# Optimization experiments

Hardware: AMD Instinct MI355X
Metric: run time of the kernel (lower is better)

The kernel has to match this reference:

```python
import jax, jax.numpy as jnp
import numpy as np

N = 100000   # nodes
E = 3200000  # edges (avg degree 32)
WIDTH = 32
DEPTH = 4


def setup_inputs() -> dict:
    key = jax.random.key(0)
    ks = jax.random.split(key, 12)
    def lin(k, fan_in, fan_out):
        s = 1.0 / np.sqrt(fan_in)
        kw, kb = jax.random.split(k)
        W = jax.random.uniform(kw, (fan_in, fan_out), jnp.float32, -s, s)
        b = jax.random.uniform(kb, (fan_out,), jnp.float32, -s, s)
        return W, b
    x = jax.random.normal(ks[0], (N, 3), jnp.float32)
    edge_index = jax.random.randint(ks[1], (2, E), 0, N, jnp.int64)
    fc1_w, fc1_b = lin(ks[2], 3, WIDTH)
    w1, b1 = lin(ks[3], WIDTH, 2 * WIDTH)
    w2, b2 = lin(ks[4], 2 * WIDTH, 2 * WIDTH)
    w3, b3 = lin(ks[5], 2 * WIDTH, WIDTH)
    fc2_w, fc2_b = lin(ks[6], WIDTH, 1)
    return {"x": x, "edge_index": edge_index,
            "fc1_w": fc1_w, "fc1_b": fc1_b,
            "w1": w1, "b1": b1, "w2": w2, "b2": b2, "w3": w3, "b3": b3,
            "fc2_w": fc2_w, "fc2_b": fc2_b}


def reference(x, edge_index, fc1_w, fc1_b, w1, b1, w2, b2, w3, b3, fc2_w, fc2_b):
    # GCNConv semantics: add self-loops, symmetric degree normalization,
    # linear transform then normalized scatter-add aggregation.
    loops = jnp.arange(N, dtype=edge_index.dtype)
    src = jnp.concatenate([edge_index[0], loops])  # [E+N]
    dst = jnp.concatenate([edge_index[1], loops])  # [E+N]
    deg = jax.ops.segment_sum(jnp.ones_like(dst, dtype=x.dtype), dst, num_segments=N)
    dinv = jnp.where(deg > 0, jax.lax.rsqrt(deg), 0.0)
    norm = (dinv[src] * dinv[dst])[:, None]  # [E+N, 1]

    def gcn(h, W, b):
        m = (h @ W)[src] * norm                      # gather + scale
        return jax.ops.segment_sum(m, dst, num_segments=N) + b  # scatter-add

    h = x @ fc1_w + fc1_b
    for _ in range(DEPTH):
        h = jax.nn.relu(gcn(h, w1, b1))
        h = jax.nn.relu(gcn(h, w2, b2))
        h = jax.nn.relu(gcn(h, w3, b3))
    return h @ fc2_w + fc2_b
```

## Files before the change

### kernel.cpp

```cpp
#include <hip/hip_runtime.h>
#include <hip/hip_fp16.h>

constexpr int NN = 100000;
constexpr int EE = 3200000;
constexpr int BLOCK = 256;
constexpr int NBINS = 782;
constexpr int BINCAP = 5120;
constexpr int CHUNK = 4096;
constexpr int NCHB = (EE + CHUNK - 1) / CHUNK;
constexpr int NCLS = 512;

typedef _Float16 h2v __attribute__((ext_vector_type(2)));

__device__ __forceinline__ float addLo(float acc, unsigned int bits) {
#if __has_builtin(__builtin_amdgcn_fdot2)
  h2v h = __builtin_bit_cast(h2v, bits);
  const h2v eLo = {(_Float16)1.0f, (_Float16)0.0f};
  return __builtin_amdgcn_fdot2(h, eLo, acc, false);
#else
  __half2 hh = __builtin_bit_cast(__half2, bits);
  return acc + __half2float(hh.x);
#endif
}

__device__ __forceinline__ float addHi(float acc, unsigned int bits) {
#if __has_builtin(__builtin_amdgcn_fdot2)
  h2v h = __builtin_bit_cast(h2v, bits);
  const h2v eHi = {(_Float16)0.0f, (_Float16)1.0f};
  return __builtin_amdgcn_fdot2(h, eHi, acc, false);
#else
  __half2 hh = __builtin_bit_cast(__half2, bits);
  return acc + __half2float(hh.y);
#endif
}

__global__ __launch_bounds__(256) void k_binA(const int* __restrict__ src,
                                              const int* __restrict__ dst,
                                              int* __restrict__ cursor,
                                              unsigned int* __restrict__ binarr) {
  __shared__ int cnt[1024];
  __shared__ int off[1024];
  __shared__ int gbase[NBINS];
  __shared__ int ssc[256];
  __shared__ unsigned int stag[CHUNK];
  int tid = threadIdx.x;
  int base = blockIdx.x * CHUNK;
  for (int i = tid; i < 1024; i += 256) cnt[i] = 0;
  __syncthreads();
  for (int i = tid; i < CHUNK; i += 256) {
    int e = base + i;
    if (e < EE) atomicAdd(&cnt[dst[e] >> 7], 1);
  }
  __syncthreads();
  int t4 = tid * 4;
  int s0 = cnt[t4], s1 = cnt[t4 + 1], s2 = cnt[t4 + 2], s3 = cnt[t4 + 3];
  int tsum = s0 + s1 + s2 + s3;
  ssc[tid] = tsum;
  __syncthreads();
  for (int o = 1; o < 256; o <<= 1) {
    int x = (tid >= o) ? ssc[tid - o] : 0;
    __syncthreads();
    ssc[tid] += x;
    __syncthreads();
  }
  int ex = ssc[tid] - tsum;
  off[t4] = ex;
  off[t4 + 1] = ex + s0;
  off[t4 + 2] = ex + s0 + s1;
  off[t4 + 3] = ex + s0 + s1 + s2;
  __syncthreads();
  for (int b = tid; b < NBINS; b += 256) {
    int c = cnt[b];
    gbase[b] = c ? atomicAdd(&cursor[b], c) : 0;
    cnt[b] = off[b];
  }
  __syncthreads();
  for (int i = tid; i < CHUNK; i += 256) {
    int e = base + i;
    if (e < EE) {
      int d = dst[e];
      int b = d >> 7;
      int p = atomicAdd(&cnt[b], 1);
      stag[p] = ((unsigned int)src[e] << 7) | (unsigned int)(d & 127);
    }
  }
  __syncthreads();
  int total = (base + CHUNK <= EE) ? CHUNK : (EE - base);
  for (int i = tid; i < total; i += 256) {
    int lo = 0, hi = NBINS - 1;
    while (lo < hi) {
      int mid = (lo + hi + 1) >> 1;
      if (off[mid] <= i) lo = mid;
      else hi = mid - 1;
    }
    binarr[(size_t)lo * BINCAP + gbase[lo] + (i - off[lo])] = stag[i];
  }
}

__global__ __launch_bounds__(256) void k_degcnt(const unsigned int* __restrict__ binarr,
                                                const int* __restrict__ cursor,
                                                int* __restrict__ deg,
                                                int* __restrict__ bh) {
  __shared__ int cnt[128];
  __shared__ int lh[NCLS];
  int b = blockIdx.x, tid = threadIdx.x;
  if (tid < 128) cnt[tid] = 0;
  for (int i = tid; i < NCLS; i += 256) lh[i] = 0;
  __syncthreads();
  int n = cursor[b];
  const unsigned int* p = binarr + (size_t)b * BINCAP;
  for (int i = tid; i < n; i += 256) atomicAdd(&cnt[p[i] & 127], 1);
  __syncthreads();
  int node = b * 128 + tid;
  if (tid < 128 && node < NN) {
    int d = cnt[tid] < NCLS ? cnt[tid] : NCLS - 1;
    deg[node] = d;
    atomicAdd(&lh[d], 1);
  }
  __syncthreads();
  for (int i = tid; i < NCLS; i += 256) bh[(size_t)i * NBINS + b] = lh[i];
}

__global__ __launch_bounds__(256) void k_rowscan(int* __restrict__ bh,
                                                 int* __restrict__ tot) {
  int wid = (blockIdx.x * 256 + threadIdx.x) >> 6;
  int lane = threadIdx.x & 63;
  if (wid >= NCLS) return;
  int* row = bh + (size_t)wid * NBINS;
  int run = 0;
  for (int base = 0; base < NBINS; base += 64) {
    int i = base + lane;
    int v = (i < NBINS) ? row[i] : 0;
    int s = v;
#pragma unroll
    for (int o = 1; o < 64; o <<= 1) {
      int x = __shfl_up(s, o);
      if (lane >= o) s += x;
    }
    if (i < NBINS) row[i] = run + s - v;
    run += __shfl(s, 63);
  }
  if (lane == 0) tot[wid] = run;
}

__global__ __launch_bounds__(NCLS) void k_clsscan(const int* __restrict__ tot,
                                                  int* __restrict__ nodestart,
                                                  int* __restrict__ edgebase) {
  __shared__ int sn[NCLS], se[NCLS];
  int t = threadIdx.x;
  int v = tot[t];
  int e0 = v * t;
  sn[t] = v;
  se[t] = e0;
  __syncthreads();
  for (int o = 1; o < NCLS; o <<= 1) {
    int a = 0, b = 0;
    if (t >= o) { a = sn[t - o]; b = se[t - o]; }
    __syncthreads();
    if (t >= o) { sn[t] += a; se[t] += b; }
    __syncthreads();
  }
  nodestart[t] = sn[t] - v;
  edgebase[t] = se[t] - e0;
}

__global__ __launch_bounds__(256) void k_place2(const int* __restrict__ deg,
                                                const int* __restrict__ bh,
                                                const int* __restrict__ nodestart,
                                                const int* __restrict__ edgebase,
                                                int* __restrict__ perm,
                                                int* __restrict__ invp,
                                                int* __restrict__ rowptr2,
                                                float* __restrict__ dinv2) {
  __shared__ int lcur[NCLS];
  int tid = threadIdx.x, b = blockIdx.x;
  for (int i = tid; i < NCLS; i += 256)
    lcur[i] = nodestart[i] + bh[(size_t)i * NBINS + b];
  __syncthreads();
  int n = b * 128 + tid;
  if (tid >= 128 || n >= NN) return;
  int d = deg[n];
  int nid = atomicAdd(&lcur[d], 1);
  perm[nid] = n;
  invp[n] = nid;
  int idx = nid - nodestart[d];
  rowptr2[nid] = edgebase[d] + idx * d;
  dinv2[nid] = rsqrtf((float)(d + 1));
  if (n == 0) rowptr2[NN] = EE;
}

__global__ __launch_bounds__(256) void k_binB2(const unsigned int* __restrict__ binarr,
                                               const int* __restrict__ cursor,
                                               const int* __restrict__ deg,
                                               const int* __restrict__ invp,
                                               const int* __restrict__ rowptr2,
                                               int* __restrict__ col2) {
  __shared__ int off[128];
  __shared__ int cur[128];
  __shared__ int nbase[128];
  __shared__ unsigned int stag[BINCAP];
  int b = blockIdx.x, tid = threadIdx.x;
  int node = b * 128 + tid;
  int d = 0;
  if (tid < 128) {
    d = (node < NN) ? deg[node] : 0;
    off[tid] = d;
  }
  __syncthreads();
  for (int o = 1; o < 128; o <<= 1) {
    int x = 0;
    if (tid < 128 && tid >= o) x = off[tid - o];
    __syncthreads();
    if (tid < 128) off[tid] += x;
    __syncthreads();
  }
  int ex = 0;
  if (tid < 128) ex = off[tid] - d;
  __syncthreads();
  if (tid < 128) {
    off[tid] = ex;
    cur[tid] = ex;
    nbase[tid] = (node < NN) ? rowptr2[invp[node]] : 0;
  }
  __syncthreads();
  int n = cursor[b];
  const unsigned int* p = binarr + (size_t)b * BINCAP;
  for (int i = tid; i < n; i += 256) {
    unsigned int e = p[i];
    int pos = atomicAdd(&cur[e & 127], 1);
    stag[pos] = e;
  }
  __syncthreads();
  for (int i = tid; i < n; i += 256) {
    unsigned int e = stag[i];
    int dl = e & 127;
    col2[nbase[dl] + (i - off[dl])] = invp[e >> 7];
  }
}

__global__ __launch_bounds__(BLOCK) void k_fc1(const float* __restrict__ x,
                                               __half* __restrict__ t0,
                                               const float* __restrict__ W,
                                               const float* __restrict__ b,
                                               const float* __restrict__ dinv,
                                               const int* __restrict__ perm) {
  __shared__ float Ws[3 * 32];
  __shared__ float bs[32];
  int tid = threadIdx.x;
  if (tid < 96) Ws[tid] = W[tid];
  if (tid < 32) bs[tid] = b[tid];
  __syncthreads();
  int node = blockIdx.x * 8 + (tid >> 5);
  int f = tid & 31;
  if (node >= NN) return;
  int on = perm[node];
  float x0 = x[on * 3], x1 = x[on * 3 + 1], x2 = x[on * 3 + 2];
  float v = fmaf(x0, Ws[f], fmaf(x1, Ws[32 + f], fmaf(x2, Ws[64 + f], bs[f])));
  t0[node * 32 + f] = __float2half(v * dinv[node]);
}

__global__ __launch_bounds__(BLOCK) void k_A(const uint2* __restrict__ t0,
                                             __half2* __restrict__ t1,
                                             const int* __restrict__ rowptr,
                                             const int* __restrict__ col,
                                             const float* __restrict__ dinv,
                                             const float* __restrict__ W1,
                                             const float* __restrict__ b1) {
  __shared__ __half2 W1h[32 * 32];
  __shared__ float b1s[64];
  __shared__ float Hs[32 * 33];
  int tid = threadIdx.x;
  for (int i = tid; i < 32 * 32; i += BLOCK) {
    int k = i >> 5, m = i & 31;
    W1h[i] = __floats2half2_rn(W1[k * 64 + 2 * m], W1[k * 64 + 2 * m + 1]);
  }
  if (tid < 64) b1s[tid] = b1[tid];
  __syncthreads();

  int tile = blockIdx.x;
  {
    int c = tid & 7, slot = tid >> 3;
    int node = tile * 32 + slot;
    uint2 raw = t0[(size_t)node * 8 + c];
    float a0 = 0.f, a1 = 0.f, a2 = 0.f, a3 = 0.f;
    a0 = addLo(a0, raw.x); a1 = addHi(a1, raw.x);
    a2 = addLo(a2, raw.y); a3 = addHi(a3, raw.y);
    int beg = rowptr[node], end = rowptr[node + 1];
#pragma unroll 8
    for (int e = beg; e < end; ++e) {
      uint2 r = t0[(size_t)col[e] * 8 + c];
      a0 = addLo(a0, r.x); a1 = addHi(a1, r.x);
      a2 = addLo(a2, r.y); a3 = addHi(a3, r.y);
    }
    float dv = dinv[node];
    Hs[slot * 33 + 4 * c] = a0 * dv;
    Hs[slot * 33 + 4 * c + 1] = a1 * dv;
    Hs[slot * 33 + 4 * c + 2] = a2 * dv;
    Hs[slot * 33 + 4 * c + 3] = a3 * dv;
  }
  __syncthreads();
  {
    int n = tid >> 3, c8 = tid & 7;
    int node = tile * 32 + n;
    float a[8];
#pragma unroll
    for (int j = 0; j < 8; ++j) a[j] = b1s[c8 * 8 + j];
#pragma unroll
    for (int k = 0; k < 32; ++k) {
      float h = Hs[n * 33 + k];
#pragma unroll
      for (int jj = 0; jj < 4; ++jj) {
        float2 w = __half22float2(W1h[k * 32 + c8 * 4 + jj]);
        a[2 * jj] = fmaf(h, w.x, a[2 * jj]);
        a[2 * jj + 1] = fmaf(h, w.y, a[2 * jj + 1]);
      }
    }
    float dv = dinv[node];
    __half2* o = t1 + (size_t)node * 32 + c8 * 4;
#pragma unroll
    for (int jj = 0; jj < 4; ++jj)
      o[jj] = __float22half2_rn(make_float2(fmaxf(a[2 * jj], 0.f) * dv,
                                            fmaxf(a[2 * jj + 1], 0.f) * dv));
  }
}

__global__ __launch_bounds__(BLOCK) void k_C(const uint2* __restrict__ t1,
                                             __half2* __restrict__ t3,
                                             const int* __restrict__ rowptr,
                                             const int* __restrict__ col,
                                             const float* __restrict__ dinv,
                                             const float* __restrict__ W2,
                                             const float* __restrict__ b2,
                                             const float* __restrict__ W3) {
  __shared__ __half2 W2h[64 * 32];
  __shared__ __half2 W3h[64 * 16];
  __shared__ float b2s[64];
  __shared__ float H2[16 * 65];
  __shared__ float G1[16 * 65];
  int tid = threadIdx.x;
  for (int i = tid; i < 64 * 32; i += BLOCK) {
    int k = i >> 5, m = i & 31;
    W2h[i] = __floats2half2_rn(W2[k * 64 + 2 * m], W2[k * 64 + 2 * m + 1]);
  }
  for (int i = tid; i < 64 * 16; i += BLOCK) {
    int k = i >> 4, m = i & 15;
    W3h[i] = __floats2half2_rn(W3[k * 32 + 2 * m], W3[k * 32 + 2 * m + 1]);
  }
  if (tid < 64) b2s[tid] = b2[tid];
  __syncthreads();

  int tile = blockIdx.x;
  {
    int c = tid & 15, slot = tid >> 4;
    int node = tile * 16 + slot;
    uint2 raw = t1[(size_t)node * 16 + c];
    float a0 = 0.f, a1 = 0.f, a2 = 0.f, a3 = 0.f;
    a0 = addLo(a0, raw.x); a1 = addHi(a1, raw.x);
    a2 = addLo(a2, raw.y); a3 = addHi(a3, raw.y);
    int beg = rowptr[node], end = rowptr[node + 1];
#pragma unroll 8
    for (int e = beg; e < end; ++e) {
      uint2 r = t1[(size_t)col[e] * 16 + c];
      a0 = addLo(a0, r.x); a1 = addHi(a1, r.x);
      a2 = addLo(a2, r.y); a3 = addHi(a3, r.y);
    }
    float dv = dinv[node];
    H2[slot * 65 + 4 * c] = a0 * dv;
    H2[slot * 65 + 4 * c + 1] = a1 * dv;
    H2[slot * 65 + 4 * c + 2] = a2 * dv;
    H2[slot * 65 + 4 * c + 3] = a3 * dv;
  }
  __syncthreads();
  {
    int n = tid >> 4, q = tid & 15;
    float a[4];
#pragma unroll
    for (int j = 0; j < 4; ++j) a[j] = b2s[q * 4 + j];
#pragma unroll
    for (int k = 0; k < 64; ++k) {
      float h = H2[n * 65 + k];
      float2 w0 = __half22float2(W2h[k * 32 + q * 2]);
      float2 w1 = __half22float2(W2h[k * 32 + q * 2 + 1]);
      a[0] = fmaf(h, w0.x, a[0]);
      a[1] = fmaf(h, w0.y, a[1]);
      a[2] = fmaf(h, w1.x, a[2]);
      a[3] = fmaf(h, w1.y, a[3]);
    }
#pragma unroll
    for (int j = 0; j < 4; ++j) G1[n * 65 + q * 4 + j] = fmaxf(a[j], 0.f);
  }
  __syncthreads();
  {
    int n = tid >> 4, c16 = tid & 15;
    int node = tile * 16 + n;
    float a0 = 0.f, a1 = 0.f;
#pragma unroll
    for (int k = 0; k < 64; ++k) {
      float h = G1[n * 65 + k];
      float2 w = __half22float2(W3h[k * 16 + c16]);
      a0 = fmaf(h, w.x, a0);
      a1 = fmaf(h, w.y, a1);
    }
    float dv = dinv[node];
    t3[(size_t)node * 16 + c16] = __float22half2_rn(make_float2(a0 * dv, a1 * dv));
  }
}

template <bool FINAL>
__global__ __launch_bounds__(BLOCK) void k_D(const uint2* __restrict__ t3,
                                             uint2* __restrict__ t0n,
                                             float* __restrict__ out,
                                             const int* __restrict__ rowptr,
                                             const int* __restrict__ col,
                                             const float* __restrict__ dinv,
                                             const float* __restrict__ b3,
                                             const float* __restrict__ fc2w,
                                             const float* __restrict__ fc2b,
                                             const int* __restrict__ perm) {
  int tid = threadIdx.x;
  int c = tid & 7, slot = tid >> 3;
  int node = blockIdx.x * 32 + slot;
  uint2 raw = t3[(size_t)node * 8 + c];
  float a0 = 0.f, a1 = 0.f, a2 = 0.f, a3 = 0.f;
  a0 = addLo(a0, raw.x); a1 = addHi(a1, raw.x);
  a2 = addLo(a2, raw.y); a3 = addHi(a3, raw.y);
  int beg = rowptr[node], end = rowptr[node + 1];
#pragma unroll 8
  for (int e = beg; e < end; ++e) {
    uint2 r = t3[(size_t)col[e] * 8 + c];
    a0 = addLo(a0, r.x); a1 = addHi(a1, r.x);
    a2 = addLo(a2, r.y); a3 = addHi(a3, r.y);
  }
  float dv = dinv[node];
  float h0 = fmaxf(fmaf(a0, dv, b3[4 * c]), 0.f);
  float h1 = fmaxf(fmaf(a1, dv, b3[4 * c + 1]), 0.f);
  float h2 = fmaxf(fmaf(a2, dv, b3[4 * c + 2]), 0.f);
  float h3 = fmaxf(fmaf(a3, dv, b3[4 * c + 3]), 0.f);
  if (!FINAL) {
    __half2 u01 = __float22half2_rn(make_float2(h0 * dv, h1 * dv));
    __half2 u23 = __float22half2_rn(make_float2(h2 * dv, h3 * dv));
    uint2 w;
    w.x = __builtin_bit_cast(unsigned int, u01);
    w.y = __builtin_bit_cast(unsigned int, u23);
    t0n[(size_t)node * 8 + c] = w;
  } else {
    float part = fmaf(h0, fc2w[4 * c],
                 fmaf(h1, fc2w[4 * c + 1],
                 fmaf(h2, fc2w[4 * c + 2], h3 * fc2w[4 * c + 3])));
#pragma unroll
    for (int off = 4; off > 0; off >>= 1) part += __shfl_down(part, off, 8);
    if (c == 0) out[perm[node]] = part + fc2b[0];
  }
}

extern "C" void kernel_launch(void* const* d_in, const int* in_sizes, int n_in,
                              void* d_out, int out_size, void* d_ws, size_t ws_size,
                              hipStream_t stream) {
  const float* x = (const float*)d_in[0];
  const int* ei = (const int*)d_in[1];
  const int* esrc = ei;
  const int* edst = ei + EE;
  const float* fc1_w = (const float*)d_in[2];
  const float* fc1_b = (const float*)d_in[3];
  const float* w1 = (const float*)d_in[4];
  const float* b1 = (const float*)d_in[5];
  const float* w2 = (const float*)d_in[6];
  const float* b2 = (const float*)d_in[7];
  const float* w3 = (const float*)d_in[8];
  const float* b3 = (const float*)d_in[9];
  const float* fc2_w = (const float*)d_in[10];
  const float* fc2_b = (const float*)d_in[11];

  char* p = (char*)d_ws;
  auto carve = [&](size_t bytes) {
    void* r = (void*)p;
    p += (bytes + 255) & ~(size_t)255;
    return r;
  };
  int* cursor = (int*)carve(NBINS * sizeof(int));
  int* nodestart = (int*)carve(NCLS * sizeof(int));
  int* edgebase = (int*)carve(NCLS * sizeof(int));
  int* tot = (int*)carve(NCLS * sizeof(int));
  int* deg = (int*)carve(NN * sizeof(int));
  int* bh = (int*)carve((size_t)NCLS * NBINS * sizeof(int));
  unsigned int* binarr = (unsigned int*)carve((size_t)NBINS * BINCAP * 4);
  int* rowptr2 = (int*)carve((NN + 1) * sizeof(int));
  int* col2 = (int*)carve(EE * sizeof(int));
  int* perm = (int*)carve(NN * sizeof(int));
  int* invp = (int*)carve(NN * sizeof(int));
  float* dinv2 = (float*)carve(NN * sizeof(float));
  __half* t32a = (__half*)carve((size_t)NN * 32 * sizeof(__half));
  __half* t64 = (__half*)carve((size_t)NN * 64 * sizeof(__half));
  __half* t32b = (__half*)carve((size_t)NN * 32 * sizeof(__half));

  hipMemsetAsync(cursor, 0, NBINS * sizeof(int), stream);

  k_binA<<<NCHB, 256, 0, stream>>>(esrc, edst, cursor, binarr);
  k_degcnt<<<NBINS, 256, 0, stream>>>(binarr, cursor, deg, bh);
  k_rowscan<<<(NCLS * 64 + 255) / 256, 256, 0, stream>>>(bh, tot);
  k_clsscan<<<1, NCLS, 0, stream>>>(tot, nodestart, edgebase);
  k_place2<<<NBINS, 256, 0, stream>>>(deg, bh, nodestart, edgebase, perm, invp,
                                      rowptr2, dinv2);
  k_binB2<<<NBINS, 256, 0, stream>>>(binarr, cursor, deg, invp, rowptr2, col2);

  k_fc1<<<NN / 8, BLOCK, 0, stream>>>(x, t32a, fc1_w, fc1_b, dinv2, perm);

  for (int it = 0; it < 4; ++it) {
    k_A<<<NN / 32, BLOCK, 0, stream>>>((const uint2*)t32a, (__half2*)t64,
                                       rowptr2, col2, dinv2, w1, b1);
    k_C<<<NN / 16, BLOCK, 0, stream>>>((const uint2*)t64, (__half2*)t32b,
                                       rowptr2, col2, dinv2, w2, b2, w3);
    if (it < 3) {
      k_D<false><<<NN / 32, BLOCK, 0, stream>>>(
          (const uint2*)t32b, (uint2*)t32a, nullptr, rowptr2, col2, dinv2, b3,
          nullptr, nullptr, nullptr);
    } else {
      k_D<true><<<NN / 32, BLOCK, 0, stream>>>(
          (const uint2*)t32b, nullptr, (float*)d_out, rowptr2, col2, dinv2, b3,
          fc2_w, fc2_b, perm);
    }
  }
}
```

Measured before the change: 678.9 us.

## Sort CSR neighbors by source bucket and launch aggregation tiles in reverse order

The CSR build now sorts each destination node's neighbor list by a coarse bucket of the permuted source index, using a two-level counting sort in shared memory. The aim is more locality in the gathers of the aggregation kernels. The aggregation kernels (A, C, D) also visit tiles in reverse block order, so the high-degree nodes, which are presumably placed last by the degree-sorted permutation, start first and the load balances better. The cost is extra shared memory (about 40KB) and more work in the one-time setup kernel.

```diff
diff --git a/kernel.cpp b/kernel.cpp
--- a/kernel.cpp
+++ b/kernel.cpp
@@ -191,50 +191,61 @@
 
 __global__ __launch_bounds__(256) void k_binB2(const unsigned int* __restrict__ binarr,
                                                const int* __restrict__ cursor,
-                                               const int* __restrict__ deg,
                                                const int* __restrict__ invp,
                                                const int* __restrict__ rowptr2,
                                                int* __restrict__ col2) {
-  __shared__ int off[128];
-  __shared__ int cur[128];
+  __shared__ unsigned int stag[BINCAP];
+  __shared__ unsigned int stag2[BINCAP];
+  __shared__ int cnt[1024];
+  __shared__ unsigned short off16[1024];
   __shared__ int nbase[128];
-  __shared__ unsigned int stag[BINCAP];
+  __shared__ int ssc[256];
   int b = blockIdx.x, tid = threadIdx.x;
-  int node = b * 128 + tid;
-  int d = 0;
-  if (tid < 128) {
-    d = (node < NN) ? deg[node] : 0;
-    off[tid] = d;
-  }
-  __syncthreads();
-  for (int o = 1; o < 128; o <<= 1) {
-    int x = 0;
-    if (tid < 128 && tid >= o) x = off[tid - o];
-    __syncthreads();
-    if (tid < 128) off[tid] += x;
-    __syncthreads();
-  }
-  int ex = 0;
-  if (tid < 128) ex = off[tid] - d;
-  __syncthreads();
-  if (tid < 128) {
-    off[tid] = ex;
-    cur[tid] = ex;
-    nbase[tid] = (node < NN) ? rowptr2[invp[node]] : 0;
-  }
-  __syncthreads();
   int n = cursor[b];
   const unsigned int* p = binarr + (size_t)b * BINCAP;
+  for (int i = tid; i < 1024; i += 256) cnt[i] = 0;
+  int node = b * 128 + tid;
+  if (tid < 128) nbase[tid] = (node < NN) ? rowptr2[invp[node]] : 0;
+  __syncthreads();
   for (int i = tid; i < n; i += 256) {
     unsigned int e = p[i];
-    int pos = atomicAdd(&cur[e & 127], 1);
-    stag[pos] = e;
-  }
+    unsigned int s = (unsigned int)invp[e >> 7];
+    stag[i] = (s << 7) | (e & 127u);
+    atomicAdd(&cnt[((e & 127u) << 3) | (s >> 14)], 1);
+  }
+  __syncthreads();
+  int t4 = tid * 4;
+  int s0 = cnt[t4], s1 = cnt[t4 + 1], s2 = cnt[t4 + 2], s3 = cnt[t4 + 3];
+  int tsum = s0 + s1 + s2 + s3;
+  ssc[tid] = tsum;
+  __syncthreads();
+  for (int o = 1; o < 256; o <<= 1) {
+    int x = (tid >= o) ? ssc[tid - o] : 0;
+    __syncthreads();
+    ssc[tid] += x;
+    __syncthreads();
+  }
+  int ex = ssc[tid] - tsum;
+  off16[t4] = (unsigned short)ex;
+  off16[t4 + 1] = (unsigned short)(ex + s0);
+  off16[t4 + 2] = (unsigned short)(ex + s0 + s1);
+  off16[t4 + 3] = (unsigned short)(ex + s0 + s1 + s2);
+  cnt[t4] = ex;
+  cnt[t4 + 1] = ex + s0;
+  cnt[t4 + 2] = ex + s0 + s1;
+  cnt[t4 + 3] = ex + s0 + s1 + s2;
   __syncthreads();
   for (int i = tid; i < n; i += 256) {
-    unsigned int e = stag[i];
-    int dl = e & 127;
-    col2[nbase[dl] + (i - off[dl])] = invp[e >> 7];
+    unsigned int en = stag[i];
+    int key = (int)(((en & 127u) << 3) | ((en >> 7) >> 14));
+    int pos = atomicAdd(&cnt[key], 1);
+    stag2[pos] = en;
+  }
+  __syncthreads();
+  for (int i = tid; i < n; i += 256) {
+    unsigned int en = stag2[i];
+    int dl = (int)(en & 127u);
+    col2[nbase[dl] + (i - (int)off16[dl << 3])] = (int)(en >> 7);
   }
 }
 
@@ -277,7 +288,7 @@
   if (tid < 64) b1s[tid] = b1[tid];
   __syncthreads();
 
-  int tile = blockIdx.x;
+  int tile = (int)gridDim.x - 1 - (int)blockIdx.x;
   {
     int c = tid & 7, slot = tid >> 3;
     int node = tile * 32 + slot;
@@ -349,7 +360,7 @@
   if (tid < 64) b2s[tid] = b2[tid];
   __syncthreads();
 
-  int tile = blockIdx.x;
+  int tile = (int)gridDim.x - 1 - (int)blockIdx.x;
   {
     int c = tid & 15, slot = tid >> 4;
     int node = tile * 16 + slot;
@@ -419,7 +430,8 @@
                                              const int* __restrict__ perm) {
   int tid = threadIdx.x;
   int c = tid & 7, slot = tid >> 3;
-  int node = blockIdx.x * 32 + slot;
+  int tile = (int)gridDim.x - 1 - (int)blockIdx.x;
+  int node = tile * 32 + slot;
   uint2 raw = t3[(size_t)node * 8 + c];
   float a0 = 0.f, a1 = 0.f, a2 = 0.f, a3 = 0.f;
   a0 = addLo(a0, raw.x); a1 = addHi(a1, raw.x);
@@ -501,7 +513,7 @@
   k_clsscan<<<1, NCLS, 0, stream>>>(tot, nodestart, edgebase);
   k_place2<<<NBINS, 256, 0, stream>>>(deg, bh, nodestart, edgebase, perm, invp,
                                       rowptr2, dinv2);
-  k_binB2<<<NBINS, 256, 0, stream>>>(binarr, cursor, deg, invp, rowptr2, col2);
+  k_binB2<<<NBINS, 256, 0, stream>>>(binarr, cursor, invp, rowptr2, col2);
 
   k_fc1<<<NN / 8, BLOCK, 0, stream>>>(x, t32a, fc1_w, fc1_b, dinv2, perm);
 
```

New measurement: 668.7 us. Within noise of the previous version (-1.5%).
